# Kernel optimization log

Measured on AMD Instinct MI355X. Metric: run time of the kernel, lower is better.

Reference implementation:

```python
import jax, jax.numpy as jnp
import numpy as np

T = 524288
INPUT_LEN = 64
N_MEMORY = 64
OUTPUT_LEN = 32


def setup_inputs() -> dict:
    key = jax.random.key(0)
    k_x, k_w1, k_b1, k_w2, k_b2 = jax.random.split(key, 5)
    s = 0.05  # tf.random_normal_initializer default stddev
    return {
        "inputs": jax.random.normal(k_x, (T, INPUT_LEN), dtype=jnp.float32),
        "W1": s * jax.random.normal(k_w1, (INPUT_LEN, 2 * N_MEMORY), dtype=jnp.float32),
        "B1": s * jax.random.normal(k_b1, (1, 2 * N_MEMORY), dtype=jnp.float32),
        "W2": s * jax.random.normal(k_w2, (N_MEMORY, OUTPUT_LEN), dtype=jnp.float32),
        "B2": s * jax.random.normal(k_b2, (1, OUTPUT_LEN), dtype=jnp.float32),
    }


def reference(inputs, W1, B1, W2, B2):
    n_memory = W2.shape[0]
    # gates: h = sigmoid(x W1 + B1), split into left/right halves  [T, M] each
    h = jax.nn.sigmoid(inputs @ W1 + B1)
    left, right = jnp.split(h, 2, axis=1)
    prod = left * right
    # affine linear recurrence: u_t = prod_{t-1} * u_{t-1} + (1 - left_{t-1}), u_0 = 0
    a = prod[:-1]            # [T-1, M] multiplicative coeffs
    b = 1.0 - left[:-1]      # [T-1, M] additive terms

    def step(u, ab):
        a_t, b_t = ab
        u = a_t * u + b_t
        return u, u

    u0 = jnp.zeros((n_memory,), dtype=inputs.dtype)
    _, us = jax.lax.scan(step, u0, (a, b))
    z = jnp.concatenate([u0[None, :], us], axis=0)  # [T, M]
    out = z @ W2 + B2                               # [T, output_len]
    return out
```

## Files before the change

### kernel.cpp

```cpp
#include <hip/hip_runtime.h>

#define TT    524288
#define CHUNK 512
#define NCH   (TT / CHUNK)
#define SUB   64
#define NSUB  (CHUNK / SUB)

typedef __attribute__((ext_vector_type(8))) short short8;
typedef __attribute__((ext_vector_type(4))) float f32x4;

__device__ __forceinline__ unsigned short f2bf(float f) {
    union { float f; unsigned u; } v; v.f = f;
    unsigned r = v.u + 0x7FFFu + ((v.u >> 16) & 1u);
    return (unsigned short)(r >> 16);
}
__device__ __forceinline__ unsigned packbf2(float a, float b) {
    union { float f; unsigned u; } va, vb; va.f = a; vb.f = b;
    unsigned ra = va.u + 0x7FFFu + ((va.u >> 16) & 1u);
    unsigned rb = vb.u + 0x7FFFu + ((vb.u >> 16) & 1u);
    return (ra >> 16) | (rb & 0xFFFF0000u);
}
__device__ __forceinline__ float2 unpackbf2(unsigned w) {
    union { unsigned u; float f; } a, b;
    a.u = w << 16; b.u = w & 0xFFFF0000u;
    return make_float2(a.f, b.f);
}
__device__ __forceinline__ float sigf(float v) {
    return __builtin_amdgcn_rcpf(1.0f + __expf(-v));
}

__global__ __launch_bounds__(256, 3)
void aphase(const float* __restrict__ x, const float* __restrict__ W1,
            const float* __restrict__ B1,
            float* __restrict__ Aout, float* __restrict__ Bout,
            uint4* __restrict__ abg)
{
    __shared__ __align__(16) short    W1t[128 * 72];
    __shared__ float    B1s[128];
    __shared__ __align__(16) short    XZ[SUB * 72];
    __shared__ unsigned abp[SUB * 65];
    __shared__ float    segA[4 * 66], segB[4 * 66];

    const int tid  = threadIdx.x;
    const int c    = blockIdx.x;
    const int wave = tid >> 6;
    const int lane = tid & 63;
    const int quad = lane >> 4;
    const int lr   = lane & 15;

    for (int i = tid; i < 2048; i += 256) {
        float4 w4 = ((const float4*)W1)[i];
        int k = i >> 5, n0 = (i & 31) * 4;
        W1t[(n0 + 0) * 72 + k] = (short)f2bf(w4.x);
        W1t[(n0 + 1) * 72 + k] = (short)f2bf(w4.y);
        W1t[(n0 + 2) * 72 + k] = (short)f2bf(w4.z);
        W1t[(n0 + 3) * 72 + k] = (short)f2bf(w4.w);
    }
    if (tid < 128) B1s[tid] = B1[tid];

    const float4* xg = (const float4*)(x + (size_t)c * CHUNK * 64);
    float4 xr0 = xg[tid], xr1 = xg[tid + 256], xr2 = xg[tid + 512], xr3 = xg[tid + 768];

    float sA = 1.0f, sB = 0.0f;

    for (int s = 0; s < NSUB; ++s) {
        {
            float4 v; int f;
#define PUTX(R, J) { v = (R); f = tid + 256 * (J); int row = f >> 4, c4 = (f & 15) * 4; \
            unsigned lo = (unsigned)f2bf(v.x) | ((unsigned)f2bf(v.y) << 16); \
            unsigned hi = (unsigned)f2bf(v.z) | ((unsigned)f2bf(v.w) << 16); \
            *(uint2*)&XZ[row * 72 + c4] = make_uint2(lo, hi); }
            PUTX(xr0, 0) PUTX(xr1, 1) PUTX(xr2, 2) PUTX(xr3, 3)
#undef PUTX
        }
        __syncthreads();

        if (s + 1 < NSUB) {
            const float4* xn = xg + (size_t)(s + 1) * 1024;
            xr0 = xn[tid]; xr1 = xn[tid + 256]; xr2 = xn[tid + 512]; xr3 = xn[tid + 768];
        }

        f32x4 acc[8];
        #pragma unroll
        for (int j = 0; j < 8; ++j) {
            float b = B1s[j * 16 + lr];
            acc[j][0] = b; acc[j][1] = b; acc[j][2] = b; acc[j][3] = b;
        }
        const short8 a0 = *(const short8*)&XZ[(wave * 16 + lr) * 72 + quad * 8];
        const short8 a1 = *(const short8*)&XZ[(wave * 16 + lr) * 72 + quad * 8 + 32];
        #pragma unroll
        for (int j = 0; j < 8; ++j) {
            const short8 b0 = *(const short8*)&W1t[(j * 16 + lr) * 72 + quad * 8];
            const short8 b1 = *(const short8*)&W1t[(j * 16 + lr) * 72 + quad * 8 + 32];
            acc[j] = __builtin_amdgcn_mfma_f32_16x16x32_bf16(a0, b0, acc[j], 0, 0, 0);
            acc[j] = __builtin_amdgcn_mfma_f32_16x16x32_bf16(a1, b1, acc[j], 0, 0, 0);
        }

        #pragma unroll
        for (int j = 0; j < 4; ++j) {
            #pragma unroll
            for (int r = 0; r < 4; ++r) {
                float hl = sigf(acc[j][r]);
                float hr = sigf(acc[j + 4][r]);
                int m = wave * 16 + quad * 4 + r;
                abp[m * 65 + j * 16 + lr] = packbf2(hl * hr, 1.0f - hl);
            }
        }
        __syncthreads();

        {
            uint4* dst = abg + ((size_t)((c * NSUB + s) * 16 + wave * 4)) * 64 + lane;
            #pragma unroll
            for (int i = 0; i < 4; ++i) {
                uint4 v;
                v.x = abp[(wave * 16 + i * 4 + 0) * 65 + lane];
                v.y = abp[(wave * 16 + i * 4 + 1) * 65 + lane];
                v.z = abp[(wave * 16 + i * 4 + 2) * 65 + lane];
                v.w = abp[(wave * 16 + i * 4 + 3) * 65 + lane];
                dst[i * 64] = v;
            }
        }

        float A = 1.0f, Bv = 0.0f;
        #pragma unroll
        for (int t = 0; t < 16; ++t) {
            float2 f2 = unpackbf2(abp[(wave * 16 + t) * 65 + lane]);
            Bv = fmaf(f2.x, Bv, f2.y); A *= f2.x;
        }
        segA[wave * 66 + lane] = A;
        segB[wave * 66 + lane] = Bv;
        __syncthreads();

        if (tid < 64) {
            #pragma unroll
            for (int q = 0; q < 4; ++q) {
                float A2 = segA[q * 66 + tid], B2v = segB[q * 66 + tid];
                sB = fmaf(A2, sB, B2v); sA *= A2;
            }
        }
    }

    if (tid < 64) { Aout[c * 64 + tid] = sA; Bout[c * 64 + tid] = sB; }
}

__global__ void carry_scan(const float* __restrict__ Aar, const float* __restrict__ Bar,
                           float* __restrict__ carry)
{
    __shared__ float sA[16 * 66], sB[16 * 66];
    const int tid = threadIdx.x;
    const int ch = tid & 63, seg = tid >> 6;
    const int c0 = seg * (NCH / 16);

    float A = 1.0f, B = 0.0f;
    #pragma unroll 8
    for (int i = 0; i < NCH / 16; ++i) {
        const int idx = c0 + i;
        const float a = Aar[idx * 64 + ch];
        const float b = Bar[idx * 64 + ch];
        B = fmaf(a, B, b); A *= a;
    }
    sA[seg * 66 + ch] = A;
    sB[seg * 66 + ch] = B;
    __syncthreads();

    float u = 0.0f;
    #pragma unroll
    for (int q = 0; q < 15; ++q)
        if (q < seg) u = fmaf(sA[q * 66 + ch], u, sB[q * 66 + ch]);
    #pragma unroll 8
    for (int i = 0; i < NCH / 16; ++i) {
        const int idx = c0 + i;
        carry[idx * 64 + ch] = u;
        u = fmaf(Aar[idx * 64 + ch], u, Bar[idx * 64 + ch]);
    }
}

__global__ __launch_bounds__(256, 4)
void ephase(const uint4* __restrict__ abg, const float* __restrict__ carry,
            const float* __restrict__ W2, const float* __restrict__ B2,
            float* __restrict__ out)
{
    __shared__ __align__(16) short Zs[SUB * 72];
    __shared__ float segA[2 * 4 * 66], segB[2 * 4 * 66];
    __shared__ __align__(16) short W2t[32 * 72];
    __shared__ float B2s[32];
    __shared__ float ucur[2 * 64];

    const int tid  = threadIdx.x;
    const int c    = blockIdx.x;
    const int wave = tid >> 6;
    const int lane = tid & 63;
    const int quad = lane >> 4;
    const int lr   = lane & 15;

    for (int i = tid; i < 512; i += 256) {
        float4 w4 = ((const float4*)W2)[i];
        int k = i >> 3, n0 = (i & 7) * 4;
        W2t[(n0 + 0) * 72 + k] = (short)f2bf(w4.x);
        W2t[(n0 + 1) * 72 + k] = (short)f2bf(w4.y);
        W2t[(n0 + 2) * 72 + k] = (short)f2bf(w4.z);
        W2t[(n0 + 3) * 72 + k] = (short)f2bf(w4.w);
    }
    if (tid < 32) B2s[tid] = B2[tid];
    if (tid < 64) ucur[tid] = carry[c * 64 + tid];

    const uint4* ag = abg + (size_t)c * (NSUB * 16 * 64);
    uint4 r0 = ag[(wave * 4 + 0) * 64 + lane];
    uint4 r1 = ag[(wave * 4 + 1) * 64 + lane];
    uint4 r2 = ag[(wave * 4 + 2) * 64 + lane];
    uint4 r3 = ag[(wave * 4 + 3) * 64 + lane];

    for (int s = 0; s < NSUB; ++s) {
        const int pb = (s & 1) * 264;
        float A = 1.0f, Bv = 0.0f; float2 f;
#define CSTEP(W) { f = unpackbf2(W); Bv = fmaf(f.x, Bv, f.y); A *= f.x; }
        CSTEP(r0.x) CSTEP(r0.y) CSTEP(r0.z) CSTEP(r0.w)
        CSTEP(r1.x) CSTEP(r1.y) CSTEP(r1.z) CSTEP(r1.w)
        CSTEP(r2.x) CSTEP(r2.y) CSTEP(r2.z) CSTEP(r2.w)
        CSTEP(r3.x) CSTEP(r3.y) CSTEP(r3.z) CSTEP(r3.w)
#undef CSTEP
        segA[pb + wave * 66 + lane] = A;
        segB[pb + wave * 66 + lane] = Bv;
        __syncthreads();

        float u = ucur[(s & 1) * 64 + lane];
        #pragma unroll
        for (int q = 0; q < 3; ++q)
            if (q < wave) u = fmaf(segA[pb + q * 66 + lane], u, segB[pb + q * 66 + lane]);

        int t = 0;
#define ESTEP(W) { Zs[(wave * 16 + t) * 72 + lane] = (short)f2bf(u); \
                   f = unpackbf2(W); u = fmaf(f.x, u, f.y); ++t; }
        ESTEP(r0.x) ESTEP(r0.y) ESTEP(r0.z) ESTEP(r0.w)
        ESTEP(r1.x) ESTEP(r1.y) ESTEP(r1.z) ESTEP(r1.w)
        ESTEP(r2.x) ESTEP(r2.y) ESTEP(r2.z) ESTEP(r2.w)
        ESTEP(r3.x) ESTEP(r3.y) ESTEP(r3.z) ESTEP(r3.w)
#undef ESTEP
        if (wave == 3) ucur[((s + 1) & 1) * 64 + lane] = u;

        if (s + 1 < NSUB) {
            const uint4* an = ag + (size_t)(s + 1) * (16 * 64);
            r0 = an[(wave * 4 + 0) * 64 + lane];
            r1 = an[(wave * 4 + 1) * 64 + lane];
            r2 = an[(wave * 4 + 2) * 64 + lane];
            r3 = an[(wave * 4 + 3) * 64 + lane];
        }

        const short8 za0 = *(const short8*)&Zs[(wave * 16 + lr) * 72 + quad * 8];
        const short8 za1 = *(const short8*)&Zs[(wave * 16 + lr) * 72 + quad * 8 + 32];
        const size_t row0g = (size_t)c * CHUNK + (size_t)s * SUB;
        #pragma unroll
        for (int nt = 0; nt < 2; ++nt) {
            f32x4 cc;
            float b = B2s[nt * 16 + lr];
            cc[0] = b; cc[1] = b; cc[2] = b; cc[3] = b;
            const short8 b0 = *(const short8*)&W2t[(nt * 16 + lr) * 72 + quad * 8];
            const short8 b1 = *(const short8*)&W2t[(nt * 16 + lr) * 72 + quad * 8 + 32];
            cc = __builtin_amdgcn_mfma_f32_16x16x32_bf16(za0, b0, cc, 0, 0, 0);
            cc = __builtin_amdgcn_mfma_f32_16x16x32_bf16(za1, b1, cc, 0, 0, 0);
            #pragma unroll
            for (int r = 0; r < 4; ++r) {
                int m = wave * 16 + quad * 4 + r;
                out[(row0g + m) * 32 + nt * 16 + lr] = cc[r];
            }
        }
    }
}

extern "C" void kernel_launch(void* const* d_in, const int* in_sizes, int n_in,
                              void* d_out, int out_size, void* d_ws, size_t ws_size,
                              hipStream_t stream)
{
    const float* x  = (const float*)d_in[0];
    const float* W1 = (const float*)d_in[1];
    const float* B1 = (const float*)d_in[2];
    const float* W2 = (const float*)d_in[3];
    const float* B2 = (const float*)d_in[4];
    float* out = (float*)d_out;

    float* Aar   = (float*)d_ws;
    float* Bar   = Aar + NCH * 64;
    float* carry = Bar + NCH * 64;
    uint4* abg   = (uint4*)(carry + NCH * 64);

    aphase<<<NCH, 256, 0, stream>>>(x, W1, B1, Aar, Bar, abg);
    carry_scan<<<1, 1024, 0, stream>>>(Aar, Bar, carry);
    ephase<<<NCH, 256, 0, stream>>>(abg, carry, W2, B2, out);
}
```

Before: 302.3 us.

## Load x fragments directly into MFMA registers and drop per-subchunk block barriers

The gate kernel now has each wave load its own 16-row fragments of x straight from global memory into registers, pack them to bf16 and feed the MFMA, skipping the shared-memory staging tile. Each wave handles 8 row-bands on its own and writes per-band scan summaries, so the three per-subchunk __syncthreads are gone and one serial combine over 32 bands runs at the end. The ab stream is written directly from registers in the layout the later kernel expects. In the output kernel the prefetch of the next subchunk's coefficients moves to the top of the loop so it overlaps the scan work. Risks are less coalesced x loads, more registers, and a longer final serial combine.

```diff
diff --git a/kernel.cpp b/kernel.cpp
--- a/kernel.cpp
+++ b/kernel.cpp
@@ -28,6 +28,8 @@
 __device__ __forceinline__ float sigf(float v) {
     return __builtin_amdgcn_rcpf(1.0f + __expf(-v));
 }
+
+union U8 { uint4 u4; short8 s8; };
 
 __global__ __launch_bounds__(256, 3)
 void aphase(const float* __restrict__ x, const float* __restrict__ W1,
@@ -35,11 +37,10 @@
             float* __restrict__ Aout, float* __restrict__ Bout,
             uint4* __restrict__ abg)
 {
-    __shared__ __align__(16) short    W1t[128 * 72];
+    __shared__ __align__(16) short W1t[128 * 72];
     __shared__ float    B1s[128];
-    __shared__ __align__(16) short    XZ[SUB * 72];
-    __shared__ unsigned abp[SUB * 65];
-    __shared__ float    segA[4 * 66], segB[4 * 66];
+    __shared__ unsigned abw[4][16 * 66];
+    __shared__ float    segA[32 * 66], segB[32 * 66];
 
     const int tid  = threadIdx.x;
     const int c    = blockIdx.x;
@@ -57,37 +58,43 @@
         W1t[(n0 + 3) * 72 + k] = (short)f2bf(w4.w);
     }
     if (tid < 128) B1s[tid] = B1[tid];
-
-    const float4* xg = (const float4*)(x + (size_t)c * CHUNK * 64);
-    float4 xr0 = xg[tid], xr1 = xg[tid + 256], xr2 = xg[tid + 512], xr3 = xg[tid + 768];
-
-    float sA = 1.0f, sB = 0.0f;
-
-    for (int s = 0; s < NSUB; ++s) {
-        {
-            float4 v; int f;
-#define PUTX(R, J) { v = (R); f = tid + 256 * (J); int row = f >> 4, c4 = (f & 15) * 4; \
-            unsigned lo = (unsigned)f2bf(v.x) | ((unsigned)f2bf(v.y) << 16); \
-            unsigned hi = (unsigned)f2bf(v.z) | ((unsigned)f2bf(v.w) << 16); \
-            *(uint2*)&XZ[row * 72 + c4] = make_uint2(lo, hi); }
-            PUTX(xr0, 0) PUTX(xr1, 1) PUTX(xr2, 2) PUTX(xr3, 3)
-#undef PUTX
-        }
-        __syncthreads();
-
-        if (s + 1 < NSUB) {
-            const float4* xn = xg + (size_t)(s + 1) * 1024;
-            xr0 = xn[tid]; xr1 = xn[tid + 256]; xr2 = xn[tid + 512]; xr3 = xn[tid + 768];
-        }
+    __syncthreads();
+
+    float bb[8];
+    #pragma unroll
+    for (int j = 0; j < 8; ++j) bb[j] = B1s[j * 16 + lr];
+
+    const float* xbase = x + (size_t)c * CHUNK * 64;
+
+    #define FRAGP(ss, rt) ((const float4*)(xbase + (size_t)(((ss) * 64 + (rt) * 16 + lr)) * 64) + quad * 2)
+
+    const float4* p0 = FRAGP(wave, 0);
+    float4 c0 = p0[0], c1 = p0[1], c2 = p0[8], c3 = p0[9];
+
+    for (int fi = 0; fi < 8; ++fi) {
+        const int ss = (fi < 4) ? wave : (wave + 4);
+        const int rt = fi & 3;
+
+        float4 n0, n1, n2, n3;
+        if (fi < 7) {
+            const int ns = (fi + 1 < 4) ? wave : (wave + 4);
+            const int nr = (fi + 1) & 3;
+            const float4* np = FRAGP(ns, nr);
+            n0 = np[0]; n1 = np[1]; n2 = np[8]; n3 = np[9];
+        }
+
+        U8 ua, ub;
+        ua.u4 = make_uint4(packbf2(c0.x, c0.y), packbf2(c0.z, c0.w),
+                           packbf2(c1.x, c1.y), packbf2(c1.z, c1.w));
+        ub.u4 = make_uint4(packbf2(c2.x, c2.y), packbf2(c2.z, c2.w),
+                           packbf2(c3.x, c3.y), packbf2(c3.z, c3.w));
+        const short8 a0 = ua.s8, a1 = ub.s8;
 
         f32x4 acc[8];
         #pragma unroll
         for (int j = 0; j < 8; ++j) {
-            float b = B1s[j * 16 + lr];
-            acc[j][0] = b; acc[j][1] = b; acc[j][2] = b; acc[j][3] = b;
-        }
-        const short8 a0 = *(const short8*)&XZ[(wave * 16 + lr) * 72 + quad * 8];
-        const short8 a1 = *(const short8*)&XZ[(wave * 16 + lr) * 72 + quad * 8 + 32];
+            acc[j][0] = bb[j]; acc[j][1] = bb[j]; acc[j][2] = bb[j]; acc[j][3] = bb[j];
+        }
         #pragma unroll
         for (int j = 0; j < 8; ++j) {
             const short8 b0 = *(const short8*)&W1t[(j * 16 + lr) * 72 + quad * 8];
@@ -96,51 +103,53 @@
             acc[j] = __builtin_amdgcn_mfma_f32_16x16x32_bf16(a1, b1, acc[j], 0, 0, 0);
         }
 
+        unsigned pk[4][4];
         #pragma unroll
         for (int j = 0; j < 4; ++j) {
             #pragma unroll
             for (int r = 0; r < 4; ++r) {
                 float hl = sigf(acc[j][r]);
                 float hr = sigf(acc[j + 4][r]);
-                int m = wave * 16 + quad * 4 + r;
-                abp[m * 65 + j * 16 + lr] = packbf2(hl * hr, 1.0f - hl);
+                pk[j][r] = packbf2(hl * hr, 1.0f - hl);
             }
         }
-        __syncthreads();
 
         {
-            uint4* dst = abg + ((size_t)((c * NSUB + s) * 16 + wave * 4)) * 64 + lane;
+            uint4* dstq = abg + ((size_t)((c * NSUB + ss) * 16 + rt * 4 + quad)) * 64 + lr;
             #pragma unroll
-            for (int i = 0; i < 4; ++i) {
-                uint4 v;
-                v.x = abp[(wave * 16 + i * 4 + 0) * 65 + lane];
-                v.y = abp[(wave * 16 + i * 4 + 1) * 65 + lane];
-                v.z = abp[(wave * 16 + i * 4 + 2) * 65 + lane];
-                v.w = abp[(wave * 16 + i * 4 + 3) * 65 + lane];
-                dst[i * 64] = v;
-            }
-        }
-
+            for (int j = 0; j < 4; ++j)
+                dstq[j * 16] = make_uint4(pk[j][0], pk[j][1], pk[j][2], pk[j][3]);
+        }
+
+        #pragma unroll
+        for (int j = 0; j < 4; ++j) {
+            #pragma unroll
+            for (int r = 0; r < 4; ++r)
+                abw[wave][(quad * 4 + r) * 66 + j * 16 + lr] = pk[j][r];
+        }
         float A = 1.0f, Bv = 0.0f;
         #pragma unroll
         for (int t = 0; t < 16; ++t) {
-            float2 f2 = unpackbf2(abp[(wave * 16 + t) * 65 + lane]);
+            float2 f2 = unpackbf2(abw[wave][t * 66 + lane]);
             Bv = fmaf(f2.x, Bv, f2.y); A *= f2.x;
         }
-        segA[wave * 66 + lane] = A;
-        segB[wave * 66 + lane] = Bv;
-        __syncthreads();
-
-        if (tid < 64) {
-            #pragma unroll
-            for (int q = 0; q < 4; ++q) {
-                float A2 = segA[q * 66 + tid], B2v = segB[q * 66 + tid];
-                sB = fmaf(A2, sB, B2v); sA *= A2;
-            }
-        }
-    }
-
-    if (tid < 64) { Aout[c * 64 + tid] = sA; Bout[c * 64 + tid] = sB; }
+        const int band = ss * 4 + rt;
+        segA[band * 66 + lane] = A;
+        segB[band * 66 + lane] = Bv;
+
+        if (fi < 7) { c0 = n0; c1 = n1; c2 = n2; c3 = n3; }
+    }
+    #undef FRAGP
+
+    __syncthreads();
+    if (tid < 64) {
+        float sA = 1.0f, sB = 0.0f;
+        for (int b = 0; b < 32; ++b) {
+            float A2 = segA[b * 66 + tid], B2v = segB[b * 66 + tid];
+            sB = fmaf(A2, sB, B2v); sA *= A2;
+        }
+        Aout[c * 64 + tid] = sA; Bout[c * 64 + tid] = sB;
+    }
 }
 
 __global__ void carry_scan(const float* __restrict__ Aar, const float* __restrict__ Bar,
@@ -212,6 +221,16 @@
 
     for (int s = 0; s < NSUB; ++s) {
         const int pb = (s & 1) * 264;
+
+        uint4 n0, n1, n2, n3;
+        if (s + 1 < NSUB) {
+            const uint4* an = ag + (size_t)(s + 1) * (16 * 64);
+            n0 = an[(wave * 4 + 0) * 64 + lane];
+            n1 = an[(wave * 4 + 1) * 64 + lane];
+            n2 = an[(wave * 4 + 2) * 64 + lane];
+            n3 = an[(wave * 4 + 3) * 64 + lane];
+        }
+
         float A = 1.0f, Bv = 0.0f; float2 f;
 #define CSTEP(W) { f = unpackbf2(W); Bv = fmaf(f.x, Bv, f.y); A *= f.x; }
         CSTEP(r0.x) CSTEP(r0.y) CSTEP(r0.z) CSTEP(r0.w)
@@ -237,14 +256,6 @@
         ESTEP(r3.x) ESTEP(r3.y) ESTEP(r3.z) ESTEP(r3.w)
 #undef ESTEP
         if (wave == 3) ucur[((s + 1) & 1) * 64 + lane] = u;
-
-        if (s + 1 < NSUB) {
-            const uint4* an = ag + (size_t)(s + 1) * (16 * 64);
-            r0 = an[(wave * 4 + 0) * 64 + lane];
-            r1 = an[(wave * 4 + 1) * 64 + lane];
-            r2 = an[(wave * 4 + 2) * 64 + lane];
-            r3 = an[(wave * 4 + 3) * 64 + lane];
-        }
 
         const short8 za0 = *(const short8*)&Zs[(wave * 16 + lr) * 72 + quad * 8];
         const short8 za1 = *(const short8*)&Zs[(wave * 16 + lr) * 72 + quad * 8 + 32];
@@ -264,6 +275,7 @@
                 out[(row0g + m) * 32 + nt * 16 + lr] = cc[r];
             }
         }
+        if (s + 1 < NSUB) { r0 = n0; r1 = n1; r2 = n2; r3 = n3; }
     }
 }
 
```

New measurement: 302.6 us. No clear change (+0.1%).
